# Performance work log

Measured on AMD Instinct MI355X. Metric: run time of the kernel, lower is better.

The kernel has to match this reference:

```python
import jax, jax.numpy as jnp
import numpy as np

N, M = 2048, 256
INPUT_DIM, EMBED_DIM, HIDDEN = 512, 256, 512


def setup_inputs() -> dict:
    key = jax.random.key(0)
    ks = jax.random.split(key, 12)
    s = 0.02
    inp = {
        "x": jax.random.normal(ks[0], (N, INPUT_DIM), dtype=jnp.float32),
        "tuples": jax.random.randint(ks[1], (M, 3), 0, 8, dtype=jnp.int64),
        # x_net: Linear(input_dim, hidden) -> ReLU -> Linear(hidden, embed_dim) -> ReLU
        "Wa": s * jax.random.normal(ks[2], (HIDDEN, INPUT_DIM), dtype=jnp.float32),
        "ba": jnp.zeros((HIDDEN,), dtype=jnp.float32),
        "Wb": s * jax.random.normal(ks[3], (EMBED_DIM, HIDDEN), dtype=jnp.float32),
        "bb": jnp.zeros((EMBED_DIM,), dtype=jnp.float32),
        # embedding tables
        "E_pred": s * jax.random.normal(ks[4], (8, EMBED_DIM), dtype=jnp.float32),
        "E_filt": s * jax.random.normal(ks[5], (192, EMBED_DIM), dtype=jnp.float32),
        "E_reo": s * jax.random.normal(ks[6], (8, EMBED_DIM), dtype=jnp.float32),
        # mlp: Linear(2*embed_dim, hidden) -> ReLU -> Linear(hidden, 1)
        "W1": s * jax.random.normal(ks[7], (HIDDEN, 2 * EMBED_DIM), dtype=jnp.float32),
        "b1": jnp.zeros((HIDDEN,), dtype=jnp.float32),
        "W2": s * jax.random.normal(ks[8], (1, HIDDEN), dtype=jnp.float32),
        "b2": jnp.zeros((1,), dtype=jnp.float32),
    }
    return inp


def reference(x, tuples, Wa, ba, Wb, bb, E_pred, E_filt, E_reo, W1, b1, W2, b2):
    # x_net: two Linear+ReLU layers -> x_emb [N, D]
    h_x = jax.nn.relu(jnp.einsum('ni,hi->nh', x, Wa) + ba)
    x_emb = jax.nn.relu(jnp.einsum('nh,dh->nd', h_x, Wb) + bb)
    # tuple embedding sum -> t_emb [M, D]
    t_emb = E_pred[tuples[:, 0]] + E_filt[tuples[:, 1]] + E_reo[tuples[:, 2]]
    # mlp first layer on concat([x_exp, t_exp]) == Wx @ x_emb + Wt @ t_emb (split W1)
    D = x_emb.shape[1]
    W1x, W1t = W1[:, :D], W1[:, D:]
    hx = jnp.einsum('nd,hd->nh', x_emb, W1x)          # [N, H]
    ht = jnp.einsum('md,hd->mh', t_emb, W1t)          # [M, H]
    h = jax.nn.relu(hx[:, None, :] + ht[None, :, :] + b1)  # [N, M, H]
    out = jnp.einsum('nmh,h->nm', h, W2[0]) + b2[0]   # [N, M]
    return out
```

## Files before the change

### kernel.cpp

```cpp
#include <hip/hip_runtime.h>

constexpr int N_     = 2048;
constexpr int IN_DIM = 512;
constexpr int HID    = 512;
constexpr int EMB    = 256;
constexpr int M_     = 256;

typedef __attribute__((ext_vector_type(8))) short short8;
typedef __attribute__((ext_vector_type(4))) float f32x4;
typedef __attribute__((ext_vector_type(2))) _Float16 h2v;

#if defined(__has_builtin)
#if __has_builtin(__builtin_amdgcn_fdot2)
#define HAVE_FDOT2 1
#endif
#endif

union U32H2 { unsigned int u; h2v v; };

__device__ __forceinline__ unsigned short f2bf(float f) {
    union { float f; unsigned int u; } v; v.f = f;
    return (unsigned short)((v.u + 0x7fffu + ((v.u >> 16) & 1u)) >> 16);
}
__device__ __forceinline__ unsigned int packh2(float a, float b) {
    U32H2 r; r.v[0] = (_Float16)a; r.v[1] = (_Float16)b; return r.u;
}
__device__ __forceinline__ h2v relu2(h2v s) {
#if defined(__has_builtin) && __has_builtin(__builtin_elementwise_max)
    U32H2 z; z.u = 0u;
    return __builtin_elementwise_max(s, z.v);
#else
    U32H2 t; t.v = s;
    const unsigned int m = ((t.u & 0x80000000u) ? 0xFFFF0000u : 0u) |
                           ((t.u & 0x00008000u) ? 0x0000FFFFu : 0u);
    t.u &= ~m;
    return t.v;
#endif
}

__global__ __launch_bounds__(256)
void prep(const float* __restrict__ x, const float* __restrict__ Wa,
          const float* __restrict__ Wb, const float* __restrict__ W1,
          const int* __restrict__ tuples, const float* __restrict__ Ep,
          const float* __restrict__ Ef, const float* __restrict__ Er,
          const float* __restrict__ w2,
          unsigned short* __restrict__ x_bf, unsigned short* __restrict__ Wa_bf,
          unsigned short* __restrict__ Wb_bf, unsigned short* __restrict__ W1x_bf,
          unsigned short* __restrict__ W1t_bf, unsigned short* __restrict__ t_emb_bf,
          unsigned int* __restrict__ w2p)
{
    const int b = blockIdx.x, t = threadIdx.x;
    if (b < 1664) {
        int q = b * 256 + t;
        float4 v; ushort4 u;
        if (q < 262144) {
            v = ((const float4*)x)[q];
            u.x = f2bf(v.x); u.y = f2bf(v.y); u.z = f2bf(v.z); u.w = f2bf(v.w);
            ((ushort4*)x_bf)[q] = u;
        } else if ((q -= 262144) < 65536) {
            v = ((const float4*)Wa)[q];
            u.x = f2bf(v.x); u.y = f2bf(v.y); u.z = f2bf(v.z); u.w = f2bf(v.w);
            ((ushort4*)Wa_bf)[q] = u;
        } else if ((q -= 65536) < 32768) {
            v = ((const float4*)Wb)[q];
            u.x = f2bf(v.x); u.y = f2bf(v.y); u.z = f2bf(v.z); u.w = f2bf(v.w);
            ((ushort4*)Wb_bf)[q] = u;
        } else {
            q -= 32768;
            v = ((const float4*)W1)[q];
            u.x = f2bf(v.x); u.y = f2bf(v.y); u.z = f2bf(v.z); u.w = f2bf(v.w);
            const int row = q >> 7, c = (q & 127) * 4;
            if (c < 256) ((ushort4*)W1x_bf)[(row * 256 + c) >> 2] = u;
            else         ((ushort4*)W1t_bf)[(row * 256 + c - 256) >> 2] = u;
        }
    } else if (b < 1728) {
        const int idx = (b - 1664) * 256 + t;
        const int m = idx >> 6, q = idx & 63;
        const int t0 = tuples[m * 3 + 0];
        const int t1 = tuples[m * 3 + 1];
        const int t2 = tuples[m * 3 + 2];
        const float4 a = ((const float4*)(Ep + t0 * EMB))[q];
        const float4 c = ((const float4*)(Ef + t1 * EMB))[q];
        const float4 d = ((const float4*)(Er + t2 * EMB))[q];
        ushort4 u;
        u.x = f2bf(a.x + c.x + d.x);
        u.y = f2bf(a.y + c.y + d.y);
        u.z = f2bf(a.z + c.z + d.z);
        u.w = f2bf(a.w + c.w + d.w);
        ((ushort4*)t_emb_bf)[m * 64 + q] = u;
    } else {
        w2p[t] = packh2(w2[2 * t], w2[2 * t + 1]);
    }
}

template<int BM, int BN, bool RELU, bool BIASC>
__global__ __launch_bounds__(256, 2)
void gemm_bf16(const unsigned short* __restrict__ A, int lda,
               const unsigned short* __restrict__ W, int ldw,
               const float* __restrict__ bias,
               unsigned short* __restrict__ Cout, int ldc, int K)
{
    constexpr int BK = 128, LDK = BK + 8;
    constexpr int SM = BM / 2, SN = BN / 2;
    constexpr int FM = SM / 16, FN = SN / 16;
    constexpr int AIT = BM / 16, WIT = BN / 16;
    __shared__ unsigned short As[2][BM][LDK];
    __shared__ unsigned short Bs[2][BN][LDK];

    const int tid  = threadIdx.x;
    const int row0 = blockIdx.x * BM, col0 = blockIdx.y * BN;
    const int wv = tid >> 6, lane = tid & 63;
    const int wr = wv >> 1, wc = wv & 1;
    const int lr = lane & 15, lq = lane >> 4;

    f32x4 acc[FM][FN];
#pragma unroll
    for (int i = 0; i < FM; ++i)
#pragma unroll
        for (int j = 0; j < FN; ++j) acc[i][j] = (f32x4)0.f;

    short8 pa[AIT], pw[WIT];
    auto issue = [&](int k0) {
#pragma unroll
        for (int i = 0; i < AIT; ++i) {
            const int idx = tid + i * 256, r = idx >> 4, c8 = idx & 15;
            pa[i] = *(const short8*)&A[(size_t)(row0 + r) * lda + k0 + c8 * 8];
        }
#pragma unroll
        for (int i = 0; i < WIT; ++i) {
            const int idx = tid + i * 256, r = idx >> 4, c8 = idx & 15;
            pw[i] = *(const short8*)&W[(size_t)(col0 + r) * ldw + k0 + c8 * 8];
        }
    };
    auto store = [&](int bsel) {
#pragma unroll
        for (int i = 0; i < AIT; ++i) {
            const int idx = tid + i * 256, r = idx >> 4, c8 = idx & 15;
            *(short8*)&As[bsel][r][c8 * 8] = pa[i];
        }
#pragma unroll
        for (int i = 0; i < WIT; ++i) {
            const int idx = tid + i * 256, r = idx >> 4, c8 = idx & 15;
            *(short8*)&Bs[bsel][r][c8 * 8] = pw[i];
        }
    };

    issue(0); store(0);
    const int NC = K / BK;
    for (int c = 0; c < NC; ++c) {
        const int buf = c & 1;
        __syncthreads();
        if (c + 1 < NC) issue((c + 1) * BK);
#pragma unroll
        for (int ks = 0; ks < BK / 32; ++ks) {
            short8 af[FM], bfr[FN];
#pragma unroll
            for (int i = 0; i < FM; ++i)
                af[i] = *(const short8*)&As[buf][wr * SM + i * 16 + lr][ks * 32 + lq * 8];
#pragma unroll
            for (int j = 0; j < FN; ++j)
                bfr[j] = *(const short8*)&Bs[buf][wc * SN + j * 16 + lr][ks * 32 + lq * 8];
#pragma unroll
            for (int i = 0; i < FM; ++i)
#pragma unroll
                for (int j = 0; j < FN; ++j)
                    acc[i][j] = __builtin_amdgcn_mfma_f32_16x16x32_bf16(
                        af[i], bfr[j], acc[i][j], 0, 0, 0);
        }
        if (c + 1 < NC) store((c + 1) & 1);
    }

#pragma unroll
    for (int i = 0; i < FM; ++i) {
#pragma unroll
        for (int j = 0; j < FN; ++j) {
            const int colb = col0 + wc * SN + j * 16 + lr;
#pragma unroll
            for (int e = 0; e < 4; ++e) {
                const int row = row0 + wr * SM + i * 16 + lq * 4 + e;
                float v = acc[i][j][e];
                if (BIASC) v += bias[colb];
                if (RELU)  v = fmaxf(v, 0.f);
                Cout[(size_t)row * ldc + colb] = f2bf(v);
            }
        }
    }
}

__global__ __launch_bounds__(256, 2)
void gemm_pair(const unsigned short* __restrict__ W1x_bf,
               const unsigned short* __restrict__ W1t_bf,
               const unsigned short* __restrict__ x_emb_bf,
               const unsigned short* __restrict__ t_emb_bf,
               const float* __restrict__ b1,
               unsigned int* __restrict__ hxT_p,
               unsigned int* __restrict__ cmT_p)
{
    constexpr int BM = 32, BN = 64, BK = 128, LDK = BK + 8;
    constexpr int SM = 16, SN = 32, FN = 2;
    __shared__ unsigned short As[2][BM][LDK];
    __shared__ unsigned short Bs[2][BN][LDK];

    const unsigned short* A; const unsigned short* B;
    const float* bias; unsigned int* outp; int ldc, col0;
    if (blockIdx.y < 32) {
        A = W1x_bf; B = x_emb_bf; bias = nullptr; outp = hxT_p;
        ldc = N_; col0 = blockIdx.y * BN;
    } else {
        A = W1t_bf; B = t_emb_bf; bias = b1; outp = cmT_p;
        ldc = M_; col0 = (blockIdx.y - 32) * BN;
    }
    const int K = EMB, row0 = blockIdx.x * BM;

    const int tid = threadIdx.x;
    const int wv = tid >> 6, lane = tid & 63;
    const int wr = wv >> 1, wc = wv & 1;
    const int lr = lane & 15, lq = lane >> 4;

    f32x4 acc[FN];
#pragma unroll
    for (int j = 0; j < FN; ++j) acc[j] = (f32x4)0.f;

    short8 pa[2], pw[4];
    auto issue = [&](int k0) {
#pragma unroll
        for (int i = 0; i < 2; ++i) {
            const int idx = tid + i * 256, r = idx >> 4, c8 = idx & 15;
            pa[i] = *(const short8*)&A[(size_t)(row0 + r) * K + k0 + c8 * 8];
        }
#pragma unroll
        for (int i = 0; i < 4; ++i) {
            const int idx = tid + i * 256, r = idx >> 4, c8 = idx & 15;
            pw[i] = *(const short8*)&B[(size_t)(col0 + r) * K + k0 + c8 * 8];
        }
    };
    auto store = [&](int bsel) {
#pragma unroll
        for (int i = 0; i < 2; ++i) {
            const int idx = tid + i * 256, r = idx >> 4, c8 = idx & 15;
            *(short8*)&As[bsel][r][c8 * 8] = pa[i];
        }
#pragma unroll
        for (int i = 0; i < 4; ++i) {
            const int idx = tid + i * 256, r = idx >> 4, c8 = idx & 15;
            *(short8*)&Bs[bsel][r][c8 * 8] = pw[i];
        }
    };

    issue(0); store(0);
    const int NC = K / BK;
    for (int c = 0; c < NC; ++c) {
        const int buf = c & 1;
        __syncthreads();
        if (c + 1 < NC) issue((c + 1) * BK);
#pragma unroll
        for (int ks = 0; ks < BK / 32; ++ks) {
            short8 af, bfr[FN];
            af = *(const short8*)&As[buf][wr * SM + lr][ks * 32 + lq * 8];
#pragma unroll
            for (int j = 0; j < FN; ++j)
                bfr[j] = *(const short8*)&Bs[buf][wc * SN + j * 16 + lr][ks * 32 + lq * 8];
#pragma unroll
            for (int j = 0; j < FN; ++j)
                acc[j] = __builtin_amdgcn_mfma_f32_16x16x32_bf16(af, bfr[j], acc[j], 0, 0, 0);
        }
        if (c + 1 < NC) store((c + 1) & 1);
    }

    const int rowb = row0 + wr * SM + lq * 4;
#pragma unroll
    for (int j = 0; j < FN; ++j) {
        const int colb = col0 + wc * SN + j * 16 + lr;
#pragma unroll
        for (int e2 = 0; e2 < 2; ++e2) {
            float v0 = acc[j][2 * e2], v1 = acc[j][2 * e2 + 1];
            if (bias) { v0 += bias[rowb + 2 * e2]; v1 += bias[rowb + 2 * e2 + 1]; }
            outp[(size_t)((rowb >> 1) + e2) * ldc + colb] = packh2(v0, v1);
        }
    }
}

__global__ __launch_bounds__(256, 2)
void fused_out(const unsigned int* __restrict__ hxT_p,
               const unsigned int* __restrict__ cmT_p,
               const unsigned int* __restrict__ w2p,
               const float* __restrict__ b2,
               float* __restrict__ out)
{
    constexpr int TN = 64, TM = 64, H2B = 64, LDT = 68;
    __shared__ unsigned int Hs[H2B][LDT];
    __shared__ unsigned int Cs[H2B][LDT];
    __shared__ unsigned int Wsh[H2B];

    const int tid = threadIdx.x;
    const int tx = tid & 15, ty = tid >> 4;
    const int n0 = blockIdx.x * TN;
    const int m0 = blockIdx.y * TM;
    const int kb = blockIdx.z * H2B;

#pragma unroll
    for (int p = 0; p < 4; ++p) {
        const int idx = tid + p * 256, r = idx >> 4, c4 = idx & 15;
        *(uint4*)&Hs[r][c4 * 4] =
            *(const uint4*)&hxT_p[(size_t)(kb + r) * N_ + n0 + c4 * 4];
        *(uint4*)&Cs[r][c4 * 4] =
            *(const uint4*)&cmT_p[(size_t)(kb + r) * M_ + m0 + c4 * 4];
    }
    if (tid < H2B) Wsh[tid] = w2p[kb + tid];
    __syncthreads();

    float acc[4][4];
#pragma unroll
    for (int i = 0; i < 4; ++i)
#pragma unroll
        for (int j = 0; j < 4; ++j) acc[i][j] = 0.f;

#ifdef HAVE_FDOT2
#pragma unroll 8
    for (int h = 0; h < H2B; ++h) {
        const uint4 av = *(const uint4*)&Hs[h][ty * 4];
        const uint4 bv = *(const uint4*)&Cs[h][tx * 4];
        U32H2 w; w.u = Wsh[h];
        U32H2 a[4], b[4];
        a[0].u = av.x; a[1].u = av.y; a[2].u = av.z; a[3].u = av.w;
        b[0].u = bv.x; b[1].u = bv.y; b[2].u = bv.z; b[3].u = bv.w;
#pragma unroll
        for (int i = 0; i < 4; ++i)
#pragma unroll
            for (int j = 0; j < 4; ++j) {
                const h2v s = relu2(a[i].v + b[j].v);
                acc[i][j] = __builtin_amdgcn_fdot2(s, w.v, acc[i][j], false);
            }
    }
#else
    U32H2 facc[4][4];
#pragma unroll
    for (int i = 0; i < 4; ++i)
#pragma unroll
        for (int j = 0; j < 4; ++j) facc[i][j].u = 0u;
#pragma unroll
    for (int hb = 0; hb < H2B / 8; ++hb) {
#pragma unroll
        for (int hh = 0; hh < 8; ++hh) {
            const int h = hb * 8 + hh;
            const uint4 av = *(const uint4*)&Hs[h][ty * 4];
            const uint4 bv = *(const uint4*)&Cs[h][tx * 4];
            U32H2 w; w.u = Wsh[h];
            U32H2 a[4], b[4];
            a[0].u = av.x; a[1].u = av.y; a[2].u = av.z; a[3].u = av.w;
            b[0].u = bv.x; b[1].u = bv.y; b[2].u = bv.z; b[3].u = bv.w;
#pragma unroll
            for (int i = 0; i < 4; ++i)
#pragma unroll
                for (int j = 0; j < 4; ++j) {
                    const h2v s = relu2(a[i].v + b[j].v);
                    facc[i][j].v = s * w.v + facc[i][j].v;
                }
        }
#pragma unroll
        for (int i = 0; i < 4; ++i)
#pragma unroll
            for (int j = 0; j < 4; ++j) {
                acc[i][j] += (float)facc[i][j].v[0] + (float)facc[i][j].v[1];
                facc[i][j].u = 0u;
            }
    }
#endif

    const float bb = (blockIdx.z == 0) ? b2[0] : 0.f;
#pragma unroll
    for (int i = 0; i < 4; ++i) {
        const int n = n0 + ty * 4 + i;
#pragma unroll
        for (int j = 0; j < 4; ++j)
            atomicAdd(&out[(size_t)n * M_ + m0 + tx * 4 + j], acc[i][j] + bb);
    }
}

extern "C" void kernel_launch(void* const* d_in, const int* in_sizes, int n_in,
                              void* d_out, int out_size, void* d_ws, size_t ws_size,
                              hipStream_t stream)
{
    const float* x      = (const float*)d_in[0];
    const int*   tuples = (const int*)d_in[1];
    const float* Wa     = (const float*)d_in[2];
    const float* ba     = (const float*)d_in[3];
    const float* Wb     = (const float*)d_in[4];
    const float* bb     = (const float*)d_in[5];
    const float* E_pred = (const float*)d_in[6];
    const float* E_filt = (const float*)d_in[7];
    const float* E_reo  = (const float*)d_in[8];
    const float* W1     = (const float*)d_in[9];
    const float* b1     = (const float*)d_in[10];
    const float* W2     = (const float*)d_in[11];
    const float* b2     = (const float*)d_in[12];
    float* out = (float*)d_out;

    char* w = (char*)d_ws;
    unsigned short* x_bf     = (unsigned short*)(w + 0);
    unsigned int*   hxT_p    = (unsigned int*)(w + 0);
    unsigned short* h_x_bf   = (unsigned short*)(w + 2097152);
    unsigned short* x_emb_bf = (unsigned short*)(w + 4194304);
    unsigned short* Wa_bf    = (unsigned short*)(w + 5242880);
    unsigned short* Wb_bf    = (unsigned short*)(w + 5767168);
    unsigned short* W1x_bf   = (unsigned short*)(w + 6029312);
    unsigned int*   cmT_p    = (unsigned int*)(w + 6291456);
    unsigned short* W1t_bf   = (unsigned short*)(w + 6553600);
    unsigned short* t_emb_bf = (unsigned short*)(w + 6815744);
    unsigned int*   w2p      = (unsigned int*)(w + 6946816);

    hipMemsetAsync(d_out, 0, (size_t)N_ * M_ * sizeof(float), stream);

    prep<<<dim3(1729), dim3(256), 0, stream>>>(
        x, Wa, Wb, W1, tuples, E_pred, E_filt, E_reo, W2,
        x_bf, Wa_bf, Wb_bf, W1x_bf, W1t_bf, t_emb_bf, w2p);

    gemm_bf16<32, 64, true, true><<<dim3(N_ / 32, HID / 64), 256, 0, stream>>>(
        x_bf, IN_DIM, Wa_bf, IN_DIM, ba, h_x_bf, HID, IN_DIM);

    gemm_bf16<32, 32, true, true><<<dim3(N_ / 32, EMB / 32), 256, 0, stream>>>(
        h_x_bf, HID, Wb_bf, HID, bb, x_emb_bf, EMB, HID);

    gemm_pair<<<dim3(HID / 32, 36), 256, 0, stream>>>(
        W1x_bf, W1t_bf, x_emb_bf, t_emb_bf, b1, hxT_p, cmT_p);

    fused_out<<<dim3(N_ / 64, M_ / 64, 4), 256, 0, stream>>>(
        hxT_p, cmT_p, w2p, b2, out);
}
```

Before: 139.8 us.

## Replace atomic split-K accumulation with fp16 partials and separate reduce kernel

The fused output kernel now splits the hidden dimension 8 ways instead of 4, with half-sized tiles and a higher occupancy hint. Each split writes fp16 partial sums to a workspace buffer instead of doing float atomicAdds into the output. A new reduce kernel sums the 8 partials, adds b2 and writes the output with vector stores, which also removes the memset. The trade is an extra launch and partial-buffer traffic, plus some precision loss from storing partials in fp16.

```diff
diff --git a/kernel.cpp b/kernel.cpp
--- a/kernel.cpp
+++ b/kernel.cpp
@@ -280,14 +280,13 @@
     }
 }
 
-__global__ __launch_bounds__(256, 2)
+__global__ __launch_bounds__(256, 4)
 void fused_out(const unsigned int* __restrict__ hxT_p,
                const unsigned int* __restrict__ cmT_p,
                const unsigned int* __restrict__ w2p,
-               const float* __restrict__ b2,
-               float* __restrict__ out)
-{
-    constexpr int TN = 64, TM = 64, H2B = 64, LDT = 68;
+               unsigned int* __restrict__ part_u32)
+{
+    constexpr int TN = 64, TM = 64, H2B = 32, LDT = 68;
     __shared__ unsigned int Hs[H2B][LDT];
     __shared__ unsigned int Cs[H2B][LDT];
     __shared__ unsigned int Wsh[H2B];
@@ -299,7 +298,7 @@
     const int kb = blockIdx.z * H2B;
 
 #pragma unroll
-    for (int p = 0; p < 4; ++p) {
+    for (int p = 0; p < 2; ++p) {
         const int idx = tid + p * 256, r = idx >> 4, c4 = idx & 15;
         *(uint4*)&Hs[r][c4 * 4] =
             *(const uint4*)&hxT_p[(size_t)(kb + r) * N_ + n0 + c4 * 4];
@@ -367,14 +366,42 @@
     }
 #endif
 
-    const float bb = (blockIdx.z == 0) ? b2[0] : 0.f;
 #pragma unroll
     for (int i = 0; i < 4; ++i) {
         const int n = n0 + ty * 4 + i;
-#pragma unroll
-        for (int j = 0; j < 4; ++j)
-            atomicAdd(&out[(size_t)n * M_ + m0 + tx * 4 + j], acc[i][j] + bb);
-    }
+        const size_t base = ((size_t)blockIdx.z * N_ + n) * (M_ / 2) + (m0 >> 1) + tx * 2;
+        part_u32[base]     = packh2(acc[i][0], acc[i][1]);
+        part_u32[base + 1] = packh2(acc[i][2], acc[i][3]);
+    }
+}
+
+__global__ __launch_bounds__(256)
+void reduce_out(const unsigned short* __restrict__ part,
+                const float* __restrict__ b2,
+                float* __restrict__ out)
+{
+    const int g = blockIdx.x * 256 + threadIdx.x;
+    const int n = g >> 5;
+    const int m0 = (g & 31) * 8;
+    const float bb = b2[0];
+    float s[8];
+#pragma unroll
+    for (int i = 0; i < 8; ++i) s[i] = bb;
+#pragma unroll
+    for (int zz = 0; zz < 8; ++zz) {
+        const uint4 v = *(const uint4*)&part[((size_t)zz * N_ + n) * M_ + m0];
+        const unsigned int vv[4] = {v.x, v.y, v.z, v.w};
+#pragma unroll
+        for (int q = 0; q < 4; ++q) {
+            U32H2 u; u.u = vv[q];
+            s[2 * q]     += (float)u.v[0];
+            s[2 * q + 1] += (float)u.v[1];
+        }
+    }
+    float4 o0 = {s[0], s[1], s[2], s[3]};
+    float4 o1 = {s[4], s[5], s[6], s[7]};
+    *(float4*)&out[(size_t)n * M_ + m0]     = o0;
+    *(float4*)&out[(size_t)n * M_ + m0 + 4] = o1;
 }
 
 extern "C" void kernel_launch(void* const* d_in, const int* in_sizes, int n_in,
@@ -397,19 +424,18 @@
     float* out = (float*)d_out;
 
     char* w = (char*)d_ws;
-    unsigned short* x_bf     = (unsigned short*)(w + 0);
-    unsigned int*   hxT_p    = (unsigned int*)(w + 0);
-    unsigned short* h_x_bf   = (unsigned short*)(w + 2097152);
-    unsigned short* x_emb_bf = (unsigned short*)(w + 4194304);
-    unsigned short* Wa_bf    = (unsigned short*)(w + 5242880);
-    unsigned short* Wb_bf    = (unsigned short*)(w + 5767168);
-    unsigned short* W1x_bf   = (unsigned short*)(w + 6029312);
-    unsigned int*   cmT_p    = (unsigned int*)(w + 6291456);
-    unsigned short* W1t_bf   = (unsigned short*)(w + 6553600);
-    unsigned short* t_emb_bf = (unsigned short*)(w + 6815744);
-    unsigned int*   w2p      = (unsigned int*)(w + 6946816);
-
-    hipMemsetAsync(d_out, 0, (size_t)N_ * M_ * sizeof(float), stream);
+    unsigned short* x_bf     = (unsigned short*)(w + (0 << 20));
+    unsigned short* h_x_bf   = (unsigned short*)(w + (2 << 20));
+    unsigned short* x_emb_bf = (unsigned short*)(w + (4 << 20));
+    unsigned short* Wa_bf    = (unsigned short*)(w + (5 << 20));
+    unsigned short* Wb_bf    = (unsigned short*)(w + (6 << 20));
+    unsigned short* W1x_bf   = (unsigned short*)(w + (7 << 20));
+    unsigned short* W1t_bf   = (unsigned short*)(w + (8 << 20));
+    unsigned short* t_emb_bf = (unsigned short*)(w + (9 << 20));
+    unsigned int*   w2p      = (unsigned int*)(w + (10 << 20));
+    unsigned int*   hxT_p    = (unsigned int*)(w + (12 << 20));
+    unsigned int*   cmT_p    = (unsigned int*)(w + (15 << 20));
+    unsigned int*   part_u32 = (unsigned int*)(w + (16 << 20));
 
     prep<<<dim3(1729), dim3(256), 0, stream>>>(
         x, Wa, Wb, W1, tuples, E_pred, E_filt, E_reo, W2,
@@ -424,6 +450,9 @@
     gemm_pair<<<dim3(HID / 32, 36), 256, 0, stream>>>(
         W1x_bf, W1t_bf, x_emb_bf, t_emb_bf, b1, hxT_p, cmT_p);
 
-    fused_out<<<dim3(N_ / 64, M_ / 64, 4), 256, 0, stream>>>(
-        hxT_p, cmT_p, w2p, b2, out);
-}
+    fused_out<<<dim3(N_ / 64, M_ / 64, 8), 256, 0, stream>>>(
+        hxT_p, cmT_p, w2p, part_u32);
+
+    reduce_out<<<dim3(65536 / 256), 256, 0, stream>>>(
+        (const unsigned short*)part_u32, b2, out);
+}
```

Result: faster. 115.2 us (-17.6%).

## Fuse fp32-to-bf16 conversion and embedding gather into GEMMs, drop atomics in output kernel

Applied to the files above, without the earlier changes.

Removes the separate prep kernel by converting fp32 inputs and weights to bf16 inside the GEMM load stage and gathering and summing the tuple embeddings inside gemm_pair. The final fused_out kernel no longer splits the hidden dimension across blocks with atomicAdd. Each block now loops over all 256 packed hidden pairs with double-buffered LDS and writes output directly, so the hipMemsetAsync goes away. This cuts two launches, a memset and atomic traffic, at the cost of reading fp32 data twice as wide in the GEMMs and fewer blocks in fused_out.

```diff
diff --git a/kernel.cpp b/kernel.cpp
--- a/kernel.cpp
+++ b/kernel.cpp
@@ -17,6 +17,7 @@
 #endif
 
 union U32H2 { unsigned int u; h2v v; };
+union S8U   { short8 s; unsigned short us[8]; };
 
 __device__ __forceinline__ unsigned short f2bf(float f) {
     union { float f; unsigned int u; } v; v.f = f;
@@ -37,68 +38,21 @@
     return t.v;
 #endif
 }
-
-__global__ __launch_bounds__(256)
-void prep(const float* __restrict__ x, const float* __restrict__ Wa,
-          const float* __restrict__ Wb, const float* __restrict__ W1,
-          const int* __restrict__ tuples, const float* __restrict__ Ep,
-          const float* __restrict__ Ef, const float* __restrict__ Er,
-          const float* __restrict__ w2,
-          unsigned short* __restrict__ x_bf, unsigned short* __restrict__ Wa_bf,
-          unsigned short* __restrict__ Wb_bf, unsigned short* __restrict__ W1x_bf,
-          unsigned short* __restrict__ W1t_bf, unsigned short* __restrict__ t_emb_bf,
-          unsigned int* __restrict__ w2p)
-{
-    const int b = blockIdx.x, t = threadIdx.x;
-    if (b < 1664) {
-        int q = b * 256 + t;
-        float4 v; ushort4 u;
-        if (q < 262144) {
-            v = ((const float4*)x)[q];
-            u.x = f2bf(v.x); u.y = f2bf(v.y); u.z = f2bf(v.z); u.w = f2bf(v.w);
-            ((ushort4*)x_bf)[q] = u;
-        } else if ((q -= 262144) < 65536) {
-            v = ((const float4*)Wa)[q];
-            u.x = f2bf(v.x); u.y = f2bf(v.y); u.z = f2bf(v.z); u.w = f2bf(v.w);
-            ((ushort4*)Wa_bf)[q] = u;
-        } else if ((q -= 65536) < 32768) {
-            v = ((const float4*)Wb)[q];
-            u.x = f2bf(v.x); u.y = f2bf(v.y); u.z = f2bf(v.z); u.w = f2bf(v.w);
-            ((ushort4*)Wb_bf)[q] = u;
-        } else {
-            q -= 32768;
-            v = ((const float4*)W1)[q];
-            u.x = f2bf(v.x); u.y = f2bf(v.y); u.z = f2bf(v.z); u.w = f2bf(v.w);
-            const int row = q >> 7, c = (q & 127) * 4;
-            if (c < 256) ((ushort4*)W1x_bf)[(row * 256 + c) >> 2] = u;
-            else         ((ushort4*)W1t_bf)[(row * 256 + c - 256) >> 2] = u;
-        }
-    } else if (b < 1728) {
-        const int idx = (b - 1664) * 256 + t;
-        const int m = idx >> 6, q = idx & 63;
-        const int t0 = tuples[m * 3 + 0];
-        const int t1 = tuples[m * 3 + 1];
-        const int t2 = tuples[m * 3 + 2];
-        const float4 a = ((const float4*)(Ep + t0 * EMB))[q];
-        const float4 c = ((const float4*)(Ef + t1 * EMB))[q];
-        const float4 d = ((const float4*)(Er + t2 * EMB))[q];
-        ushort4 u;
-        u.x = f2bf(a.x + c.x + d.x);
-        u.y = f2bf(a.y + c.y + d.y);
-        u.z = f2bf(a.z + c.z + d.z);
-        u.w = f2bf(a.w + c.w + d.w);
-        ((ushort4*)t_emb_bf)[m * 64 + q] = u;
-    } else {
-        w2p[t] = packh2(w2[2 * t], w2[2 * t + 1]);
-    }
-}
-
-template<int BM, int BN, bool RELU, bool BIASC>
+__device__ __forceinline__ short8 cvt8(const float4& f0, const float4& f1) {
+    S8U t;
+    t.us[0] = f2bf(f0.x); t.us[1] = f2bf(f0.y);
+    t.us[2] = f2bf(f0.z); t.us[3] = f2bf(f0.w);
+    t.us[4] = f2bf(f1.x); t.us[5] = f2bf(f1.y);
+    t.us[6] = f2bf(f1.z); t.us[7] = f2bf(f1.w);
+    return t.s;
+}
+
+template<int BM, int BN, bool ACVT>
 __global__ __launch_bounds__(256, 2)
-void gemm_bf16(const unsigned short* __restrict__ A, int lda,
-               const unsigned short* __restrict__ W, int ldw,
-               const float* __restrict__ bias,
-               unsigned short* __restrict__ Cout, int ldc, int K)
+void gemm_cvt(const void* __restrict__ Ap, int lda,
+              const float* __restrict__ Wf, int ldw,
+              const float* __restrict__ bias,
+              unsigned short* __restrict__ Cout, int ldc, int K)
 {
     constexpr int BK = 128, LDK = BK + 8;
     constexpr int SM = BM / 2, SN = BN / 2;
@@ -119,29 +73,40 @@
 #pragma unroll
         for (int j = 0; j < FN; ++j) acc[i][j] = (f32x4)0.f;
 
-    short8 pa[AIT], pw[WIT];
+    float4 paf[AIT][2];
+    short8 pab[AIT];
+    float4 pwf[WIT][2];
+
     auto issue = [&](int k0) {
 #pragma unroll
         for (int i = 0; i < AIT; ++i) {
             const int idx = tid + i * 256, r = idx >> 4, c8 = idx & 15;
-            pa[i] = *(const short8*)&A[(size_t)(row0 + r) * lda + k0 + c8 * 8];
+            if (ACVT) {
+                const float* A = (const float*)Ap;
+                paf[i][0] = *(const float4*)&A[(size_t)(row0 + r) * lda + k0 + c8 * 8];
+                paf[i][1] = *(const float4*)&A[(size_t)(row0 + r) * lda + k0 + c8 * 8 + 4];
+            } else {
+                const unsigned short* A = (const unsigned short*)Ap;
+                pab[i] = *(const short8*)&A[(size_t)(row0 + r) * lda + k0 + c8 * 8];
+            }
         }
 #pragma unroll
         for (int i = 0; i < WIT; ++i) {
             const int idx = tid + i * 256, r = idx >> 4, c8 = idx & 15;
-            pw[i] = *(const short8*)&W[(size_t)(col0 + r) * ldw + k0 + c8 * 8];
+            pwf[i][0] = *(const float4*)&Wf[(size_t)(col0 + r) * ldw + k0 + c8 * 8];
+            pwf[i][1] = *(const float4*)&Wf[(size_t)(col0 + r) * ldw + k0 + c8 * 8 + 4];
         }
     };
     auto store = [&](int bsel) {
 #pragma unroll
         for (int i = 0; i < AIT; ++i) {
             const int idx = tid + i * 256, r = idx >> 4, c8 = idx & 15;
-            *(short8*)&As[bsel][r][c8 * 8] = pa[i];
+            *(short8*)&As[bsel][r][c8 * 8] = ACVT ? cvt8(paf[i][0], paf[i][1]) : pab[i];
         }
 #pragma unroll
         for (int i = 0; i < WIT; ++i) {
             const int idx = tid + i * 256, r = idx >> 4, c8 = idx & 15;
-            *(short8*)&Bs[bsel][r][c8 * 8] = pw[i];
+            *(short8*)&Bs[bsel][r][c8 * 8] = cvt8(pwf[i][0], pwf[i][1]);
         }
     };
 
@@ -178,9 +143,7 @@
 #pragma unroll
             for (int e = 0; e < 4; ++e) {
                 const int row = row0 + wr * SM + i * 16 + lq * 4 + e;
-                float v = acc[i][j][e];
-                if (BIASC) v += bias[colb];
-                if (RELU)  v = fmaxf(v, 0.f);
+                float v = fmaxf(acc[i][j][e] + bias[colb], 0.f);
                 Cout[(size_t)row * ldc + colb] = f2bf(v);
             }
         }
@@ -188,11 +151,11 @@
 }
 
 __global__ __launch_bounds__(256, 2)
-void gemm_pair(const unsigned short* __restrict__ W1x_bf,
-               const unsigned short* __restrict__ W1t_bf,
+void gemm_pair(const float* __restrict__ W1,
                const unsigned short* __restrict__ x_emb_bf,
-               const unsigned short* __restrict__ t_emb_bf,
-               const float* __restrict__ b1,
+               const int* __restrict__ tuples,
+               const float* __restrict__ Ep, const float* __restrict__ Ef,
+               const float* __restrict__ Er, const float* __restrict__ b1,
                unsigned int* __restrict__ hxT_p,
                unsigned int* __restrict__ cmT_p)
 {
@@ -201,18 +164,15 @@
     __shared__ unsigned short As[2][BM][LDK];
     __shared__ unsigned short Bs[2][BN][LDK];
 
-    const unsigned short* A; const unsigned short* B;
-    const float* bias; unsigned int* outp; int ldc, col0;
-    if (blockIdx.y < 32) {
-        A = W1x_bf; B = x_emb_bf; bias = nullptr; outp = hxT_p;
-        ldc = N_; col0 = blockIdx.y * BN;
-    } else {
-        A = W1t_bf; B = t_emb_bf; bias = b1; outp = cmT_p;
-        ldc = M_; col0 = (blockIdx.y - 32) * BN;
-    }
-    const int K = EMB, row0 = blockIdx.x * BM;
-
     const int tid = threadIdx.x;
+    const bool gat = (blockIdx.y >= 32);
+    const int col0 = (gat ? (int)blockIdx.y - 32 : (int)blockIdx.y) * BN;
+    const int ldc  = gat ? M_ : N_;
+    unsigned int* outp = gat ? cmT_p : hxT_p;
+    const int xoff = gat ? EMB : 0;
+    const int row0 = blockIdx.x * BM;
+    const int K = EMB;
+
     const int wv = tid >> 6, lane = tid & 63;
     const int wr = wv >> 1, wc = wv & 1;
     const int lr = lane & 15, lq = lane >> 4;
@@ -221,29 +181,52 @@
 #pragma unroll
     for (int j = 0; j < FN; ++j) acc[j] = (f32x4)0.f;
 
-    short8 pa[2], pw[4];
+    float4 paf[2][2];
+    short8 pb[4];
+    float4 pbf[4][2];
+
     auto issue = [&](int k0) {
 #pragma unroll
         for (int i = 0; i < 2; ++i) {
             const int idx = tid + i * 256, r = idx >> 4, c8 = idx & 15;
-            pa[i] = *(const short8*)&A[(size_t)(row0 + r) * K + k0 + c8 * 8];
+            const size_t base = (size_t)(row0 + r) * (2 * EMB) + xoff + k0 + c8 * 8;
+            paf[i][0] = *(const float4*)&W1[base];
+            paf[i][1] = *(const float4*)&W1[base + 4];
         }
 #pragma unroll
         for (int i = 0; i < 4; ++i) {
             const int idx = tid + i * 256, r = idx >> 4, c8 = idx & 15;
-            pw[i] = *(const short8*)&B[(size_t)(col0 + r) * K + k0 + c8 * 8];
+            if (!gat) {
+                pb[i] = *(const short8*)&x_emb_bf[(size_t)(col0 + r) * EMB + k0 + c8 * 8];
+            } else {
+                const int mr = col0 + r;
+                const int t0 = tuples[mr * 3 + 0];
+                const int t1 = tuples[mr * 3 + 1];
+                const int t2 = tuples[mr * 3 + 2];
+                const int base = k0 + c8 * 8;
+                const float4 a0 = *(const float4*)&Ep[t0 * EMB + base];
+                const float4 a1 = *(const float4*)&Ep[t0 * EMB + base + 4];
+                const float4 b0 = *(const float4*)&Ef[t1 * EMB + base];
+                const float4 b1v = *(const float4*)&Ef[t1 * EMB + base + 4];
+                const float4 c0 = *(const float4*)&Er[t2 * EMB + base];
+                const float4 c1 = *(const float4*)&Er[t2 * EMB + base + 4];
+                pbf[i][0].x = a0.x + b0.x + c0.x;  pbf[i][0].y = a0.y + b0.y + c0.y;
+                pbf[i][0].z = a0.z + b0.z + c0.z;  pbf[i][0].w = a0.w + b0.w + c0.w;
+                pbf[i][1].x = a1.x + b1v.x + c1.x; pbf[i][1].y = a1.y + b1v.y + c1.y;
+                pbf[i][1].z = a1.z + b1v.z + c1.z; pbf[i][1].w = a1.w + b1v.w + c1.w;
+            }
         }
     };
     auto store = [&](int bsel) {
 #pragma unroll
         for (int i = 0; i < 2; ++i) {
             const int idx = tid + i * 256, r = idx >> 4, c8 = idx & 15;
-            *(short8*)&As[bsel][r][c8 * 8] = pa[i];
+            *(short8*)&As[bsel][r][c8 * 8] = cvt8(paf[i][0], paf[i][1]);
         }
 #pragma unroll
         for (int i = 0; i < 4; ++i) {
             const int idx = tid + i * 256, r = idx >> 4, c8 = idx & 15;
-            *(short8*)&Bs[bsel][r][c8 * 8] = pw[i];
+            *(short8*)&Bs[bsel][r][c8 * 8] = gat ? cvt8(pbf[i][0], pbf[i][1]) : pb[i];
         }
     };
 
@@ -274,7 +257,7 @@
 #pragma unroll
         for (int e2 = 0; e2 < 2; ++e2) {
             float v0 = acc[j][2 * e2], v1 = acc[j][2 * e2 + 1];
-            if (bias) { v0 += bias[rowb + 2 * e2]; v1 += bias[rowb + 2 * e2 + 1]; }
+            if (gat) { v0 += b1[rowb + 2 * e2]; v1 += b1[rowb + 2 * e2 + 1]; }
             outp[(size_t)((rowb >> 1) + e2) * ldc + colb] = packh2(v0, v1);
         }
     }
@@ -283,97 +266,105 @@
 __global__ __launch_bounds__(256, 2)
 void fused_out(const unsigned int* __restrict__ hxT_p,
                const unsigned int* __restrict__ cmT_p,
-               const unsigned int* __restrict__ w2p,
+               const float* __restrict__ w2,
                const float* __restrict__ b2,
                float* __restrict__ out)
 {
-    constexpr int TN = 64, TM = 64, H2B = 64, LDT = 68;
-    __shared__ unsigned int Hs[H2B][LDT];
-    __shared__ unsigned int Cs[H2B][LDT];
-    __shared__ unsigned int Wsh[H2B];
+    constexpr int TN = 64, TM = 32, KC = 64, NCH = 256 / KC;
+    constexpr int LDH = 72, LDC = 40;
+    __shared__ unsigned int Hs[2][KC][LDH];
+    __shared__ unsigned int Cs[2][KC][LDC];
+    __shared__ unsigned int Wsh[256];
 
     const int tid = threadIdx.x;
     const int tx = tid & 15, ty = tid >> 4;
     const int n0 = blockIdx.x * TN;
     const int m0 = blockIdx.y * TM;
-    const int kb = blockIdx.z * H2B;
-
-#pragma unroll
-    for (int p = 0; p < 4; ++p) {
-        const int idx = tid + p * 256, r = idx >> 4, c4 = idx & 15;
-        *(uint4*)&Hs[r][c4 * 4] =
-            *(const uint4*)&hxT_p[(size_t)(kb + r) * N_ + n0 + c4 * 4];
-        *(uint4*)&Cs[r][c4 * 4] =
-            *(const uint4*)&cmT_p[(size_t)(kb + r) * M_ + m0 + c4 * 4];
-    }
-    if (tid < H2B) Wsh[tid] = w2p[kb + tid];
-    __syncthreads();
-
-    float acc[4][4];
-#pragma unroll
-    for (int i = 0; i < 4; ++i)
-#pragma unroll
-        for (int j = 0; j < 4; ++j) acc[i][j] = 0.f;
-
+
+    Wsh[tid] = packh2(w2[2 * tid], w2[2 * tid + 1]);
+
+    uint4 ph[4], pc[2];
+    auto issue = [&](int kb) {
+#pragma unroll
+        for (int p = 0; p < 4; ++p) {
+            const int idx = tid + p * 256, r = idx >> 4, c4 = idx & 15;
+            ph[p] = *(const uint4*)&hxT_p[(size_t)(kb + r) * N_ + n0 + c4 * 4];
+        }
+#pragma unroll
+        for (int p = 0; p < 2; ++p) {
+            const int idx = tid + p * 256, r = idx >> 3, c4 = idx & 7;
+            pc[p] = *(const uint4*)&cmT_p[(size_t)(kb + r) * M_ + m0 + c4 * 4];
+        }
+    };
+    auto store = [&](int b) {
+#pragma unroll
+        for (int p = 0; p < 4; ++p) {
+            const int idx = tid + p * 256, r = idx >> 4, c4 = idx & 15;
+            *(uint4*)&Hs[b][r][c4 * 4] = ph[p];
+        }
+#pragma unroll
+        for (int p = 0; p < 2; ++p) {
+            const int idx = tid + p * 256, r = idx >> 3, c4 = idx & 7;
+            *(uint4*)&Cs[b][r][c4 * 4] = pc[p];
+        }
+    };
+
+    float acc[4][2];
+#pragma unroll
+    for (int i = 0; i < 4; ++i) { acc[i][0] = 0.f; acc[i][1] = 0.f; }
+
+#ifndef HAVE_FDOT2
+    U32H2 facc[4][2];
+#pragma unroll
+    for (int i = 0; i < 4; ++i) { facc[i][0].u = 0u; facc[i][1].u = 0u; }
+#endif
+
+    issue(0); store(0);
+    for (int c = 0; c < NCH; ++c) {
+        const int buf = c & 1;
+        __syncthreads();
+        if (c + 1 < NCH) issue((c + 1) * KC);
+#pragma unroll 8
+        for (int h = 0; h < KC; ++h) {
+            const uint4 av = *(const uint4*)&Hs[buf][h][ty * 4];
+            const uint2 bv = *(const uint2*)&Cs[buf][h][tx * 2];
+            U32H2 w; w.u = Wsh[c * KC + h];
+            U32H2 a[4], b[2];
+            a[0].u = av.x; a[1].u = av.y; a[2].u = av.z; a[3].u = av.w;
+            b[0].u = bv.x; b[1].u = bv.y;
+#pragma unroll
+            for (int i = 0; i < 4; ++i)
+#pragma unroll
+                for (int j = 0; j < 2; ++j) {
+                    const h2v s = relu2(a[i].v + b[j].v);
 #ifdef HAVE_FDOT2
-#pragma unroll 8
-    for (int h = 0; h < H2B; ++h) {
-        const uint4 av = *(const uint4*)&Hs[h][ty * 4];
-        const uint4 bv = *(const uint4*)&Cs[h][tx * 4];
-        U32H2 w; w.u = Wsh[h];
-        U32H2 a[4], b[4];
-        a[0].u = av.x; a[1].u = av.y; a[2].u = av.z; a[3].u = av.w;
-        b[0].u = bv.x; b[1].u = bv.y; b[2].u = bv.z; b[3].u = bv.w;
-#pragma unroll
-        for (int i = 0; i < 4; ++i)
-#pragma unroll
-            for (int j = 0; j < 4; ++j) {
-                const h2v s = relu2(a[i].v + b[j].v);
-                acc[i][j] = __builtin_amdgcn_fdot2(s, w.v, acc[i][j], false);
+                    acc[i][j] = __builtin_amdgcn_fdot2(s, w.v, acc[i][j], false);
+#else
+                    facc[i][j].v = s * w.v + facc[i][j].v;
+#endif
+                }
+#ifndef HAVE_FDOT2
+            if ((h & 7) == 7) {
+#pragma unroll
+                for (int i = 0; i < 4; ++i)
+#pragma unroll
+                    for (int j = 0; j < 2; ++j) {
+                        acc[i][j] += (float)facc[i][j].v[0] + (float)facc[i][j].v[1];
+                        facc[i][j].u = 0u;
+                    }
             }
-    }
-#else
-    U32H2 facc[4][4];
-#pragma unroll
-    for (int i = 0; i < 4; ++i)
-#pragma unroll
-        for (int j = 0; j < 4; ++j) facc[i][j].u = 0u;
-#pragma unroll
-    for (int hb = 0; hb < H2B / 8; ++hb) {
-#pragma unroll
-        for (int hh = 0; hh < 8; ++hh) {
-            const int h = hb * 8 + hh;
-            const uint4 av = *(const uint4*)&Hs[h][ty * 4];
-            const uint4 bv = *(const uint4*)&Cs[h][tx * 4];
-            U32H2 w; w.u = Wsh[h];
-            U32H2 a[4], b[4];
-            a[0].u = av.x; a[1].u = av.y; a[2].u = av.z; a[3].u = av.w;
-            b[0].u = bv.x; b[1].u = bv.y; b[2].u = bv.z; b[3].u = bv.w;
-#pragma unroll
-            for (int i = 0; i < 4; ++i)
-#pragma unroll
-                for (int j = 0; j < 4; ++j) {
-                    const h2v s = relu2(a[i].v + b[j].v);
-                    facc[i][j].v = s * w.v + facc[i][j].v;
-                }
-        }
-#pragma unroll
-        for (int i = 0; i < 4; ++i)
-#pragma unroll
-            for (int j = 0; j < 4; ++j) {
-                acc[i][j] += (float)facc[i][j].v[0] + (float)facc[i][j].v[1];
-                facc[i][j].u = 0u;
-            }
-    }
-#endif
-
-    const float bb = (blockIdx.z == 0) ? b2[0] : 0.f;
+#endif
+        }
+        if (c + 1 < NCH) store((c + 1) & 1);
+    }
+
+    const float bb = b2[0];
 #pragma unroll
     for (int i = 0; i < 4; ++i) {
-        const int n = n0 + ty * 4 + i;
-#pragma unroll
-        for (int j = 0; j < 4; ++j)
-            atomicAdd(&out[(size_t)n * M_ + m0 + tx * 4 + j], acc[i][j] + bb);
+        float2 o;
+        o.x = acc[i][0] + bb;
+        o.y = acc[i][1] + bb;
+        *(float2*)&out[(size_t)(n0 + ty * 4 + i) * M_ + m0 + tx * 2] = o;
     }
 }
 
@@ -397,33 +388,20 @@
     float* out = (float*)d_out;
 
     char* w = (char*)d_ws;
-    unsigned short* x_bf     = (unsigned short*)(w + 0);
-    unsigned int*   hxT_p    = (unsigned int*)(w + 0);
-    unsigned short* h_x_bf   = (unsigned short*)(w + 2097152);
-    unsigned short* x_emb_bf = (unsigned short*)(w + 4194304);
-    unsigned short* Wa_bf    = (unsigned short*)(w + 5242880);
-    unsigned short* Wb_bf    = (unsigned short*)(w + 5767168);
-    unsigned short* W1x_bf   = (unsigned short*)(w + 6029312);
-    unsigned int*   cmT_p    = (unsigned int*)(w + 6291456);
-    unsigned short* W1t_bf   = (unsigned short*)(w + 6553600);
-    unsigned short* t_emb_bf = (unsigned short*)(w + 6815744);
-    unsigned int*   w2p      = (unsigned int*)(w + 6946816);
-
-    hipMemsetAsync(d_out, 0, (size_t)N_ * M_ * sizeof(float), stream);
-
-    prep<<<dim3(1729), dim3(256), 0, stream>>>(
-        x, Wa, Wb, W1, tuples, E_pred, E_filt, E_reo, W2,
-        x_bf, Wa_bf, Wb_bf, W1x_bf, W1t_bf, t_emb_bf, w2p);
-
-    gemm_bf16<32, 64, true, true><<<dim3(N_ / 32, HID / 64), 256, 0, stream>>>(
-        x_bf, IN_DIM, Wa_bf, IN_DIM, ba, h_x_bf, HID, IN_DIM);
-
-    gemm_bf16<32, 32, true, true><<<dim3(N_ / 32, EMB / 32), 256, 0, stream>>>(
-        h_x_bf, HID, Wb_bf, HID, bb, x_emb_bf, EMB, HID);
+    unsigned short* h_x_bf   = (unsigned short*)(w + (0 << 20));
+    unsigned short* x_emb_bf = (unsigned short*)(w + (4 << 20));
+    unsigned int*   hxT_p    = (unsigned int*)(w + (8 << 20));
+    unsigned int*   cmT_p    = (unsigned int*)(w + (12 << 20));
+
+    gemm_cvt<32, 64, true><<<dim3(N_ / 32, HID / 64), 256, 0, stream>>>(
+        x, IN_DIM, Wa, IN_DIM, ba, h_x_bf, HID, IN_DIM);
+
+    gemm_cvt<32, 32, false><<<dim3(N_ / 32, EMB / 32), 256, 0, stream>>>(
+        h_x_bf, HID, Wb, HID, bb, x_emb_bf, EMB, HID);
 
     gemm_pair<<<dim3(HID / 32, 36), 256, 0, stream>>>(
-        W1x_bf, W1t_bf, x_emb_bf, t_emb_bf, b1, hxT_p, cmT_p);
-
-    fused_out<<<dim3(N_ / 64, M_ / 64, 4), 256, 0, stream>>>(
-        hxT_p, cmT_p, w2p, b2, out);
-}
+        W1, x_emb_bf, tuples, E_pred, E_filt, E_reo, b1, hxT_p, cmT_p);
+
+    fused_out<<<dim3(N_ / 64, M_ / 32), 256, 0, stream>>>(
+        hxT_p, cmT_p, W2, b2, out);
+}
```

Result: faster. 132.6 us (-5.1%).
